# Kernel tuning notes

Measured on AMD Instinct MI355X. Metric: run time of the kernel, lower is better.

## Reference

```python
import jax, jax.numpy as jnp
import numpy as np
from jax import lax

TTQ_THRESHOLD_FACTOR = 0.05


def ttq_quantize(w, wp, wn, t):
    # w: [O,I,k,k]; wp, wn: [1] (already abs'ed); t: scalar threshold
    mask_pos = w > t
    mask_neg = w < -t
    return mask_pos.astype(w.dtype) * wp[0] - mask_neg.astype(w.dtype) * wn[0]


def setup_inputs() -> dict:
    key = jax.random.key(0)
    k1, k2, k3 = jax.random.split(key, 3)
    B, Cin, H, W = 64, 128, 56, 56
    Cout, K = 256, 3
    x = jax.random.normal(k1, (B, Cin, H, W), dtype=jnp.float32)
    # kaiming-uniform-ish init scale; exact init distribution does not matter for math
    weight = jax.random.normal(k2, (Cout, Cin, K, K), dtype=jnp.float32) * 0.05
    bias = jax.random.normal(k3, (Cout,), dtype=jnp.float32) * 0.01
    wp = jnp.full((1,), 0.1, dtype=jnp.float32)
    wn = jnp.full((1,), 0.1, dtype=jnp.float32)
    return {"x": x, "weight": weight, "bias": bias, "wp": wp, "wn": wn}


def reference(x, weight, bias, wp, wn):
    # threshold computed on detached weight
    t = TTQ_THRESHOLD_FACTOR * jnp.max(jnp.abs(lax.stop_gradient(weight)))
    qw = ttq_quantize(weight, jnp.abs(wp), jnp.abs(wn), t)
    out = lax.conv_general_dilated(
        x, qw,
        window_strides=(1, 1), padding="VALID",
        dimension_numbers=("NCHW", "OIHW", "NCHW"),
    )
    return out + bias[None, :, None, None]
```

## Files before the change

kernel.cpp:

```cpp
#include <hip/hip_runtime.h>
#include <hip/hip_bf16.h>

#define BATCH 64
#define CIN   128
#define HIN   56
#define WIN   56
#define COUT  256
#define KSZ   3
#define OHP   54
#define OWP   54
#define NSPAT (OHP * OWP)
#define NTILES 23
#define KDIM  (CIN * KSZ * KSZ)

typedef short bf16x8 __attribute__((ext_vector_type(8)));
typedef float f32x4  __attribute__((ext_vector_type(4)));

static __device__ __forceinline__ unsigned short f2bf(float f) {
    unsigned v = __float_as_uint(f);
    v += 0x7FFFu + ((v >> 16) & 1u);
    return (unsigned short)(v >> 16);
}

static __device__ __forceinline__ void gl_lds16(const void* g, void* l) {
    __builtin_amdgcn_global_load_lds(
        (const __attribute__((address_space(1))) void*)g,
        (__attribute__((address_space(3))) void*)l, 16, 0, 0);
}

__global__ __launch_bounds__(256) void maxabs_kernel(const float* __restrict__ w,
                                                     float* __restrict__ blockmax, int n) {
    float m = 0.f;
    for (int i = blockIdx.x * 256 + threadIdx.x; i < n; i += gridDim.x * 256)
        m = fmaxf(m, fabsf(w[i]));
    for (int off = 32; off > 0; off >>= 1)
        m = fmaxf(m, __shfl_down(m, off));
    __shared__ float red[4];
    if ((threadIdx.x & 63) == 0) red[threadIdx.x >> 6] = m;
    __syncthreads();
    if (threadIdx.x == 0)
        blockmax[blockIdx.x] = fmaxf(fmaxf(red[0], red[1]), fmaxf(red[2], red[3]));
}

__global__ __launch_bounds__(256) void quant_kernel(const float* __restrict__ w,
                                                    const float* __restrict__ wp,
                                                    const float* __restrict__ wn,
                                                    const float* __restrict__ blockmax,
                                                    unsigned short* __restrict__ qw) {
    __shared__ float red[4];
    float m = blockmax[threadIdx.x];
    for (int off = 32; off > 0; off >>= 1)
        m = fmaxf(m, __shfl_down(m, off));
    if ((threadIdx.x & 63) == 0) red[threadIdx.x >> 6] = m;
    __syncthreads();
    float t = 0.05f * fmaxf(fmaxf(red[0], red[1]), fmaxf(red[2], red[3]));

    int idx = blockIdx.x * 256 + threadIdx.x;
    float p = fabsf(wp[0]), nn = fabsf(wn[0]);
    float v = w[idx];
    float q = (v > t) ? p : ((v < -t) ? -nn : 0.0f);
    int co  = idx / KDIM;
    int rem = idx - co * KDIM;
    int ci  = rem / 9;
    int kk  = rem - ci * 9;
    qw[co * KDIM + kk * CIN + ci] = f2bf(q);
}

__global__ __launch_bounds__(256) void cast_nhwc_kernel(const float* __restrict__ x,
                                                        unsigned short* __restrict__ xt) {
    int b = blockIdx.x / HIN;
    int h = blockIdx.x - b * HIN;
    __shared__ __align__(16) unsigned short xsb[56][136];

    for (int t = threadIdx.x; t < 448; t += 256) {
        int cig = t / 14, wg = t - cig * 14;
        int ci0 = cig * 4, w0 = wg * 4;
        const float* xp = x + ((size_t)(b * CIN + ci0) * HIN + h) * WIN + w0;
        float4 v0 = *(const float4*)(xp);
        float4 v1 = *(const float4*)(xp + (size_t)HIN * WIN);
        float4 v2 = *(const float4*)(xp + 2 * (size_t)HIN * WIN);
        float4 v3 = *(const float4*)(xp + 3 * (size_t)HIN * WIN);
        float a0[4] = {v0.x, v0.y, v0.z, v0.w};
        float a1[4] = {v1.x, v1.y, v1.z, v1.w};
        float a2[4] = {v2.x, v2.y, v2.z, v2.w};
        float a3[4] = {v3.x, v3.y, v3.z, v3.w};
#pragma unroll
        for (int k = 0; k < 4; ++k) {
            uint2 u;
            u.x = (unsigned)f2bf(a0[k]) | ((unsigned)f2bf(a1[k]) << 16);
            u.y = (unsigned)f2bf(a2[k]) | ((unsigned)f2bf(a3[k]) << 16);
            *(uint2*)&xsb[w0 + k][ci0] = u;
        }
    }
    __syncthreads();

    for (int id = threadIdx.x; id < 896; id += 256) {
        int w_ = id >> 4, cq = id & 15;
        uint4 val = *(const uint4*)&xsb[w_][cq * 8];
        *(uint4*)&xt[((size_t)(b * HIN + h) * WIN + w_) * CIN + cq * 8] = val;
    }
}

__global__ __launch_bounds__(256, 3) void conv_mfma_kernel(const unsigned short* __restrict__ xt,
                                                           const unsigned short* __restrict__ qw,
                                                           const float* __restrict__ bias,
                                                           float* __restrict__ out) {
    int xcd = blockIdx.x & 7;
    int k   = blockIdx.x >> 3;
    int g   = k / 46;
    int r   = k - g * 46;
    int b   = g * 8 + xcd;
    int mt  = r / 23;
    int nt  = r - mt * 23;

    __shared__ __align__(16) unsigned short As[128 * 64];
    __shared__ __align__(16) unsigned short Bs[128 * 64];

    int t    = threadIdx.x;
    int wave = t >> 6, lane = t & 63;
    int wm   = wave >> 1, wcol = wave & 1;
    int quad = lane >> 4, r16 = lane & 15;

    int row0 = t >> 3;
    int lc   = (t & 7) ^ (row0 & 7);

    const unsigned short* Ab = qw + (size_t)(mt * 128 + row0) * KDIM + lc * 8;
    const unsigned short* Bb[4];
#pragma unroll
    for (int c = 0; c < 4; ++c) {
        unsigned n = nt * 128 + c * 32 + row0;
        if (n > NSPAT - 1) n = NSPAT - 1;
        unsigned oh = n / OWP, ow = n - oh * OWP;
        Bb[c] = xt + ((size_t)(b * HIN + oh) * WIN + ow) * CIN + lc * 8;
    }

    f32x4 acc[4][4] = {};

#pragma unroll
    for (int kk = 0; kk < 18; ++kk) {
        int slice = kk >> 1;
        int kh = slice / 3, kw = slice - kh * 3;
        int boff = (kh * WIN + kw) * CIN + (kk & 1) * 64;
        int aoff = kk * 64;

#pragma unroll
        for (int c = 0; c < 4; ++c) {
            gl_lds16(Ab + aoff + c * 32 * KDIM, (char*)As + c * 4096 + wave * 1024);
            gl_lds16(Bb[c] + boff,              (char*)Bs + c * 4096 + wave * 1024);
        }
        __syncthreads();

#pragma unroll
        for (int s = 0; s < 2; ++s) {
            int pc = ((s * 4 + quad) ^ (r16 & 7)) * 8;
            bf16x8 af[4], bfr[4];
#pragma unroll
            for (int i = 0; i < 4; ++i)
                af[i] = *(const bf16x8*)&As[(wm * 64 + i * 16 + r16) * 64 + pc];
#pragma unroll
            for (int j = 0; j < 4; ++j)
                bfr[j] = *(const bf16x8*)&Bs[(wcol * 64 + j * 16 + r16) * 64 + pc];
#pragma unroll
            for (int i = 0; i < 4; ++i)
#pragma unroll
                for (int j = 0; j < 4; ++j)
                    acc[i][j] = __builtin_amdgcn_mfma_f32_16x16x32_bf16(af[i], bfr[j], acc[i][j], 0, 0, 0);
        }
        __syncthreads();
    }

#pragma unroll
    for (int i = 0; i < 4; ++i) {
        int co_base = mt * 128 + wm * 64 + i * 16 + quad * 4;
        float4 bv = *(const float4*)(bias + co_base);
        float bvd[4] = {bv.x, bv.y, bv.z, bv.w};
#pragma unroll
        for (int d = 0; d < 4; ++d) {
            size_t rowb = (size_t)(b * COUT + co_base + d) * NSPAT;
#pragma unroll
            for (int j = 0; j < 4; ++j) {
                unsigned n = nt * 128 + wcol * 64 + j * 16 + r16;
                if (n < NSPAT)
                    out[rowb + n] = acc[i][j][d] + bvd[d];
            }
        }
    }
}

extern "C" void kernel_launch(void* const* d_in, const int* in_sizes, int n_in,
                              void* d_out, int out_size, void* d_ws, size_t ws_size,
                              hipStream_t stream) {
    const float* x      = (const float*)d_in[0];
    const float* weight = (const float*)d_in[1];
    const float* bias   = (const float*)d_in[2];
    const float* wp     = (const float*)d_in[3];
    const float* wn     = (const float*)d_in[4];
    float* out          = (float*)d_out;

    float*          bmax = (float*)d_ws;
    unsigned short* qw   = (unsigned short*)((char*)d_ws + 1024);
    unsigned short* xt   = (unsigned short*)((char*)d_ws + 590848);

    maxabs_kernel<<<256, 256, 0, stream>>>(weight, bmax, COUT * KDIM);
    quant_kernel<<<(COUT * KDIM) / 256, 256, 0, stream>>>(weight, wp, wn, bmax, qw);
    cast_nhwc_kernel<<<BATCH * HIN, 256, 0, stream>>>(x, xt);
    conv_mfma_kernel<<<2 * BATCH * NTILES, 256, 0, stream>>>(xt, qw, bias, out);
}
```

Baseline: 387.0 us.

## Flatten batch and spatial into one N dimension with 128x192 tiles

The conv GEMM now treats batch and output pixels as one flat N dimension. It uses 192-wide N tiles (6 MFMA column fragments per wave instead of 4), so there are no partial tiles per image and the A tile is reused across more columns. Block IDs are remapped so consecutive tiles land on the same XCD. The kernel gains more accumulator registers and 24KB of B LDS, which may lower occupancy under launch_bounds(256,3). Output rows can now span image boundaries and need per-column batch/offset math.

```diff
diff --git a/kernel.cpp b/kernel.cpp
--- a/kernel.cpp
+++ b/kernel.cpp
@@ -10,8 +10,10 @@
 #define OHP   54
 #define OWP   54
 #define NSPAT (OHP * OWP)
-#define NTILES 23
+#define NFLAT (BATCH * NSPAT)
 #define KDIM  (CIN * KSZ * KSZ)
+#define NTILE 972
+#define NBLK2 1944
 
 typedef short bf16x8 __attribute__((ext_vector_type(8)));
 typedef float f32x4  __attribute__((ext_vector_type(4)));
@@ -105,36 +107,34 @@
                                                            const unsigned short* __restrict__ qw,
                                                            const float* __restrict__ bias,
                                                            float* __restrict__ out) {
-    int xcd = blockIdx.x & 7;
-    int k   = blockIdx.x >> 3;
-    int g   = k / 46;
-    int r   = k - g * 46;
-    int b   = g * 8 + xcd;
-    int mt  = r / 23;
-    int nt  = r - mt * 23;
+    unsigned orig = blockIdx.x;
+    unsigned wgid = (orig & 7u) * 243u + (orig >> 3);
+    int mt    = wgid / NTILE;
+    int ntile = wgid - mt * NTILE;
+    unsigned n0 = ntile * 192u;
 
     __shared__ __align__(16) unsigned short As[128 * 64];
-    __shared__ __align__(16) unsigned short Bs[128 * 64];
+    __shared__ __align__(16) unsigned short Bs[192 * 64];
 
     int t    = threadIdx.x;
     int wave = t >> 6, lane = t & 63;
     int wm   = wave >> 1, wcol = wave & 1;
     int quad = lane >> 4, r16 = lane & 15;
 
-    int row0 = t >> 3;
-    int lc   = (t & 7) ^ (row0 & 7);
-
-    const unsigned short* Ab = qw + (size_t)(mt * 128 + row0) * KDIM + lc * 8;
-    const unsigned short* Bb[4];
-#pragma unroll
-    for (int c = 0; c < 4; ++c) {
-        unsigned n = nt * 128 + c * 32 + row0;
-        if (n > NSPAT - 1) n = NSPAT - 1;
-        unsigned oh = n / OWP, ow = n - oh * OWP;
-        Bb[c] = xt + ((size_t)(b * HIN + oh) * WIN + ow) * CIN + lc * 8;
-    }
-
-    f32x4 acc[4][4] = {};
+    int row_s = t >> 3;
+    int lc    = (t & 7) ^ (row_s & 7);
+
+    const unsigned short* Ab = qw + (size_t)(mt * 128 + row_s) * KDIM + lc * 8;
+    const unsigned short* Bg[6];
+#pragma unroll
+    for (int c = 0; c < 6; ++c) {
+        unsigned n = n0 + c * 32 + row_s;
+        unsigned b = n / NSPAT, rem = n - b * NSPAT;
+        unsigned oh = rem / OWP, ow = rem - oh * OWP;
+        Bg[c] = xt + ((size_t)((b * HIN + oh) * WIN + ow)) * CIN + lc * 8;
+    }
+
+    f32x4 acc[4][6] = {};
 
 #pragma unroll
     for (int kk = 0; kk < 18; ++kk) {
@@ -144,31 +144,38 @@
         int aoff = kk * 64;
 
 #pragma unroll
-        for (int c = 0; c < 4; ++c) {
+        for (int c = 0; c < 4; ++c)
             gl_lds16(Ab + aoff + c * 32 * KDIM, (char*)As + c * 4096 + wave * 1024);
-            gl_lds16(Bb[c] + boff,              (char*)Bs + c * 4096 + wave * 1024);
-        }
+#pragma unroll
+        for (int c = 0; c < 6; ++c)
+            gl_lds16(Bg[c] + boff,              (char*)Bs + c * 4096 + wave * 1024);
         __syncthreads();
 
 #pragma unroll
         for (int s = 0; s < 2; ++s) {
             int pc = ((s * 4 + quad) ^ (r16 & 7)) * 8;
-            bf16x8 af[4], bfr[4];
+            bf16x8 af[4], bfr[6];
 #pragma unroll
             for (int i = 0; i < 4; ++i)
                 af[i] = *(const bf16x8*)&As[(wm * 64 + i * 16 + r16) * 64 + pc];
 #pragma unroll
-            for (int j = 0; j < 4; ++j)
-                bfr[j] = *(const bf16x8*)&Bs[(wcol * 64 + j * 16 + r16) * 64 + pc];
+            for (int j = 0; j < 6; ++j)
+                bfr[j] = *(const bf16x8*)&Bs[(wcol * 96 + j * 16 + r16) * 64 + pc];
 #pragma unroll
             for (int i = 0; i < 4; ++i)
 #pragma unroll
-                for (int j = 0; j < 4; ++j)
+                for (int j = 0; j < 6; ++j)
                     acc[i][j] = __builtin_amdgcn_mfma_f32_16x16x32_bf16(af[i], bfr[j], acc[i][j], 0, 0, 0);
         }
         __syncthreads();
     }
 
+    unsigned bj[6], rj[6];
+#pragma unroll
+    for (int j = 0; j < 6; ++j) {
+        unsigned n = n0 + wcol * 96 + j * 16 + r16;
+        bj[j] = n / NSPAT; rj[j] = n - bj[j] * NSPAT;
+    }
 #pragma unroll
     for (int i = 0; i < 4; ++i) {
         int co_base = mt * 128 + wm * 64 + i * 16 + quad * 4;
@@ -176,13 +183,10 @@
         float bvd[4] = {bv.x, bv.y, bv.z, bv.w};
 #pragma unroll
         for (int d = 0; d < 4; ++d) {
-            size_t rowb = (size_t)(b * COUT + co_base + d) * NSPAT;
-#pragma unroll
-            for (int j = 0; j < 4; ++j) {
-                unsigned n = nt * 128 + wcol * 64 + j * 16 + r16;
-                if (n < NSPAT)
-                    out[rowb + n] = acc[i][j][d] + bvd[d];
-            }
+#pragma unroll
+            for (int j = 0; j < 6; ++j)
+                out[((size_t)(bj[j] * COUT + co_base + d)) * NSPAT + rj[j]] =
+                    acc[i][j][d] + bvd[d];
         }
     }
 }
@@ -204,5 +208,5 @@
     maxabs_kernel<<<256, 256, 0, stream>>>(weight, bmax, COUT * KDIM);
     quant_kernel<<<(COUT * KDIM) / 256, 256, 0, stream>>>(weight, wp, wn, bmax, qw);
     cast_nhwc_kernel<<<BATCH * HIN, 256, 0, stream>>>(x, xt);
-    conv_mfma_kernel<<<2 * BATCH * NTILES, 256, 0, stream>>>(xt, qw, bias, out);
-}
+    conv_mfma_kernel<<<NBLK2, 256, 0, stream>>>(xt, qw, bias, out);
+}
```

Result: no change. 384.3 us (-0.7%).
